# Performance work log

Hardware: AMD Instinct MI355X
Metric: run time of the kernel (lower is better)

Reference implementation:

```python
import jax, jax.numpy as jnp
import numpy as np

D = 256       # hp.encoder_dim
F = 256       # hp.duration_predictor_filter_size
K = 3         # hp.duration_predictor_kernel_size
ALPHA = 1.0
EPS = 1e-5


def _conv1d(x, w):
    # x: [N, L, Cin], w: [K, Cin, Cout], 'same' padding=1 for K=3
    return jax.lax.conv_general_dilated(
        x, w, window_strides=(1,), padding=((1, 1),),
        dimension_numbers=('NWC', 'WIO', 'NWC'))


def _layer_norm(h, g, b):
    mu = jnp.mean(h, axis=-1, keepdims=True)
    var = jnp.var(h, axis=-1, keepdims=True)
    return (h - mu) * jax.lax.rsqrt(var + EPS) * g + b


def setup_inputs() -> dict:
    key = jax.random.key(0)
    ks = jax.random.split(key, 12)
    N, L = 16, 512
    xavier_cw = float(np.sqrt(2.0 / (D * K + F * K)))  # xavier-ish for conv
    xavier_lw = float(np.sqrt(2.0 / (F + 1)))
    return {
        'x': jax.random.normal(ks[0], (N, L, D), dtype=jnp.float32),
        'conv1_w': jax.random.normal(ks[1], (K, D, F), dtype=jnp.float32) * xavier_cw,
        'conv1_b': jnp.zeros((F,), dtype=jnp.float32),
        'ln1_g': jnp.ones((F,), dtype=jnp.float32),
        'ln1_b': jnp.zeros((F,), dtype=jnp.float32),
        'conv2_w': jax.random.normal(ks[2], (K, F, F), dtype=jnp.float32) * xavier_cw,
        'conv2_b': jnp.zeros((F,), dtype=jnp.float32),
        'ln2_g': jnp.ones((F,), dtype=jnp.float32),
        'ln2_b': jnp.zeros((F,), dtype=jnp.float32),
        'lin_w': jax.random.normal(ks[3], (F, 1), dtype=jnp.float32) * xavier_lw,
        'lin_b': jnp.zeros((1,), dtype=jnp.float32),
        'WVF_max_length': 4096,
    }


def reference(x, conv1_w, conv1_b, ln1_g, ln1_b, conv2_w, conv2_b,
              ln2_g, ln2_b, lin_w, lin_b, WVF_max_length):
    # ---- DurationPredictor (eval mode: dropout = identity) ----
    h = _conv1d(x, conv1_w) + conv1_b            # [N, L, F]
    h = jax.nn.relu(_layer_norm(h, ln1_g, ln1_b))
    h = _conv1d(h, conv2_w) + conv2_b
    h = jax.nn.relu(_layer_norm(h, ln2_g, ln2_b))
    dpo = jax.nn.relu(h @ lin_w + lin_b)[..., 0]  # [N, L]

    # ---- LengthRegulator (no attn): int durations, alignment @ x ----
    dur = ((dpo + 0.5) * ALPHA).astype(jnp.int32)  # [N, L]
    ends = jnp.cumsum(dur, axis=-1)                # inclusive cumsum
    starts = ends - dur                            # exclusive cumsum
    t = jnp.arange(WVF_max_length)                 # static output length
    # alignment[n, t, l] = 1 iff starts[n,l] <= t < ends[n,l]
    align = ((t[None, :, None] >= starts[:, None, :]) &
             (t[None, :, None] < ends[:, None, :])).astype(x.dtype)  # [N, T, L]
    out = jnp.einsum('ntl,nld->ntd', align, x)     # [N, T, D]

    WVF_pos = jnp.arange(1, WVF_max_length + 1, dtype=jnp.int64
                         if jax.config.jax_enable_x64 else jnp.int32)[None, :]
    return out, WVF_pos
```

## Files before the change

kernel.cpp:

```cpp
#include <hip/hip_runtime.h>
#include <math.h>

#define N_   16
#define L_   512
#define C_   256
#define T_   4096
#define EPSL 1e-5f
#define BM   32

typedef short short8 __attribute__((ext_vector_type(8)));
typedef float f32x4  __attribute__((ext_vector_type(4)));

__device__ __forceinline__ ushort f2bf(float f) {
    union { float f; unsigned u; } v; v.f = f;
    return (ushort)((v.u + 0x7FFF + ((v.u >> 16) & 1)) >> 16);
}

__global__ __launch_bounds__(256) void pack_w_kernel(
    const float* __restrict__ w1, const float* __restrict__ w2,
    ushort* __restrict__ bpk1, ushort* __restrict__ bpk2,
    float* __restrict__ wpos)
{
    int gid = blockIdx.x * 256 + threadIdx.x;
    if (gid < T_) wpos[gid] = (float)(gid + 1);
    const float* w  = (gid < 24576) ? w1 : w2;
    ushort* bpk     = (gid < 24576) ? bpk1 : bpk2;
    int g2 = gid & 24575;
    int lane = g2 & 63;
    int s    = (g2 >> 6) & 7;
    int cg   = (g2 >> 9) & 15;
    int karm = g2 >> 13;
    int cin0 = s * 32 + (lane >> 4) * 8;
    int cout = cg * 16 + (lane & 15);
    const float* src = w + (size_t)(karm * 256 + cin0) * 256 + cout;
    short8 o;
    #pragma unroll
    for (int e = 0; e < 8; ++e) o[e] = (short)f2bf(src[(size_t)e * 256]);
    *reinterpret_cast<short8*>(bpk + (size_t)g2 * 8) = o;
}

__global__ __launch_bounds__(512, 4) void fused_conv_kernel(
    const float* __restrict__ x,
    const ushort* __restrict__ bpk1, const ushort* __restrict__ bpk2,
    const float* __restrict__ b1, const float* __restrict__ g1, const float* __restrict__ be1,
    const float* __restrict__ b2, const float* __restrict__ g2, const float* __restrict__ be2,
    const float* __restrict__ lw, const float* __restrict__ lb,
    int* __restrict__ dur)
{
    __shared__ __align__(16) char xt[50 * 512];
    __shared__ __align__(16) char h1t[34 * 512];
    __shared__ float redS[8][48], redQ[8][48], redP[8][32];

    const int tid  = threadIdx.x;
    const int wv   = tid >> 6;
    const int lane = tid & 63;
    const int lg   = lane >> 4;
    const int lr   = lane & 15;
    const int n    = blockIdx.x >> 4;
    const int l0   = (blockIdx.x & 15) << 5;
    const int cg0  = wv * 2;
    const int col0 = wv * 32 + lr, col1 = col0 + 16;

    for (int idx = tid; idx < 36 * 32; idx += 512) {
        int r = idx >> 5, slot = idx & 31;
        int l = l0 - 2 + r;
        short8 vb = {0,0,0,0,0,0,0,0};
        if (l >= 0 && l < L_) {
            const float* src = x + (((size_t)(n * L_ + l)) << 8) + (slot << 3);
            f32x4 f0 = *reinterpret_cast<const f32x4*>(src);
            f32x4 f1 = *reinterpret_cast<const f32x4*>(src + 4);
            vb[0]=(short)f2bf(f0[0]); vb[1]=(short)f2bf(f0[1]);
            vb[2]=(short)f2bf(f0[2]); vb[3]=(short)f2bf(f0[3]);
            vb[4]=(short)f2bf(f1[0]); vb[5]=(short)f2bf(f1[1]);
            vb[6]=(short)f2bf(f1[2]); vb[7]=(short)f2bf(f1[3]);
        }
        *reinterpret_cast<short8*>(xt + r * 512 + ((slot ^ (r & 15)) << 4)) = vb;
    }
    __syncthreads();

    f32x4 a1t[3][2] = {};
    #pragma unroll
    for (int karm = 0; karm < 3; ++karm) {
        const ushort* bb = bpk1 + ((size_t)(karm * 16 + cg0)) * 4096 + lane * 8;
        #pragma unroll
        for (int half = 0; half < 2; ++half) {
            short8 bf0[4], bf1[4];
            #pragma unroll
            for (int s4 = 0; s4 < 4; ++s4) {
                int s = half * 4 + s4;
                bf0[s4] = *reinterpret_cast<const short8*>(bb + s * 512);
                bf1[s4] = *reinterpret_cast<const short8*>(bb + 4096 + s * 512);
            }
            #pragma unroll
            for (int s4 = 0; s4 < 4; ++s4) {
                int s = half * 4 + s4;
                #pragma unroll
                for (int t = 0; t < 3; ++t) {
                    int rA = 16 * t + lr + karm;
                    short8 a = *reinterpret_cast<const short8*>(
                        xt + rA * 512 + ((((s << 2) + lg) ^ (rA & 15)) << 4));
                    a1t[t][0] = __builtin_amdgcn_mfma_f32_16x16x32_bf16(a, bf0[s4], a1t[t][0], 0, 0, 0);
                    a1t[t][1] = __builtin_amdgcn_mfma_f32_16x16x32_bf16(a, bf1[s4], a1t[t][1], 0, 0, 0);
                }
            }
        }
    }

    const float cb10 = b1[col0], cb11 = b1[col1];
    const float cg10 = g1[col0], cg11 = g1[col1];
    const float ce10 = be1[col0], ce11 = be1[col1];
    {
        float sv[12], qv[12];
        #pragma unroll
        for (int t = 0; t < 3; ++t)
            #pragma unroll
            for (int j = 0; j < 4; ++j) {
                float h0 = a1t[t][0][j] + cb10, h1 = a1t[t][1][j] + cb11;
                sv[t*4+j] = h0 + h1; qv[t*4+j] = h0 * h0 + h1 * h1;
            }
        #pragma unroll
        for (int m = 1; m < 16; m <<= 1)
            #pragma unroll
            for (int k = 0; k < 12; ++k) {
                sv[k] += __shfl_xor(sv[k], m, 64);
                qv[k] += __shfl_xor(qv[k], m, 64);
            }
        if (lr == 0) {
            #pragma unroll
            for (int t = 0; t < 3; ++t)
                #pragma unroll
                for (int j = 0; j < 4; ++j) {
                    redS[wv][16*t + lg*4 + j] = sv[t*4+j];
                    redQ[wv][16*t + lg*4 + j] = qv[t*4+j];
                }
        }
    }
    __syncthreads();
    if (tid < 48) {
        float ss = 0.f, qq = 0.f;
        #pragma unroll
        for (int u = 0; u < 8; ++u) { ss += redS[u][tid]; qq += redQ[u][tid]; }
        float m_  = ss * (1.f / 256.f);
        float var = fmaxf(qq * (1.f / 256.f) - m_ * m_, 0.f);
        redS[0][tid] = m_;
        redQ[0][tid] = 1.0f / sqrtf(var + EPSL);
    }
    __syncthreads();

    #pragma unroll
    for (int t = 0; t < 3; ++t)
        #pragma unroll
        for (int j = 0; j < 4; ++j) {
            int hr = 16*t + lg*4 + j;
            if (hr < 34) {
                int hl = l0 - 1 + hr;
                float r0 = 0.f, r1 = 0.f;
                if (hl >= 0 && hl < L_) {
                    r0 = fmaxf((a1t[t][0][j] + cb10 - redS[0][hr]) * redQ[0][hr] * cg10 + ce10, 0.f);
                    r1 = fmaxf((a1t[t][1][j] + cb11 - redS[0][hr]) * redQ[0][hr] * cg11 + ce11, 0.f);
                }
                *(ushort*)(h1t + hr*512 + (((col0 >> 3) ^ (hr & 15)) << 4) + (col0 & 7) * 2) = f2bf(r0);
                *(ushort*)(h1t + hr*512 + (((col1 >> 3) ^ (hr & 15)) << 4) + (col1 & 7) * 2) = f2bf(r1);
            }
        }
    __syncthreads();

    f32x4 c2[2][2] = {};
    #pragma unroll
    for (int karm = 0; karm < 3; ++karm) {
        const ushort* bb = bpk2 + ((size_t)(karm * 16 + cg0)) * 4096 + lane * 8;
        #pragma unroll
        for (int half = 0; half < 2; ++half) {
            short8 bf0[4], bf1[4];
            #pragma unroll
            for (int s4 = 0; s4 < 4; ++s4) {
                int s = half * 4 + s4;
                bf0[s4] = *reinterpret_cast<const short8*>(bb + s * 512);
                bf1[s4] = *reinterpret_cast<const short8*>(bb + 4096 + s * 512);
            }
            #pragma unroll
            for (int s4 = 0; s4 < 4; ++s4) {
                int s = half * 4 + s4;
                #pragma unroll
                for (int tt = 0; tt < 2; ++tt) {
                    int rA = 16 * tt + lr + karm;
                    short8 a = *reinterpret_cast<const short8*>(
                        h1t + rA * 512 + ((((s << 2) + lg) ^ (rA & 15)) << 4));
                    c2[tt][0] = __builtin_amdgcn_mfma_f32_16x16x32_bf16(a, bf0[s4], c2[tt][0], 0, 0, 0);
                    c2[tt][1] = __builtin_amdgcn_mfma_f32_16x16x32_bf16(a, bf1[s4], c2[tt][1], 0, 0, 0);
                }
            }
        }
    }

    const float cb20 = b2[col0], cb21 = b2[col1];
    const float cg20 = g2[col0], cg21 = g2[col1];
    const float ce20 = be2[col0], ce21 = be2[col1];
    const float lw0  = lw[col0],  lw1  = lw[col1];
    {
        float sv[8], qv[8];
        #pragma unroll
        for (int tt = 0; tt < 2; ++tt)
            #pragma unroll
            for (int j = 0; j < 4; ++j) {
                float h0 = c2[tt][0][j] + cb20, h1 = c2[tt][1][j] + cb21;
                sv[tt*4+j] = h0 + h1; qv[tt*4+j] = h0 * h0 + h1 * h1;
            }
        #pragma unroll
        for (int m = 1; m < 16; m <<= 1)
            #pragma unroll
            for (int k = 0; k < 8; ++k) {
                sv[k] += __shfl_xor(sv[k], m, 64);
                qv[k] += __shfl_xor(qv[k], m, 64);
            }
        if (lr == 0) {
            #pragma unroll
            for (int tt = 0; tt < 2; ++tt)
                #pragma unroll
                for (int j = 0; j < 4; ++j) {
                    redS[wv][16*tt + lg*4 + j] = sv[tt*4+j];
                    redQ[wv][16*tt + lg*4 + j] = qv[tt*4+j];
                }
        }
    }
    __syncthreads();
    if (tid < 32) {
        float ss = 0.f, qq = 0.f;
        #pragma unroll
        for (int u = 0; u < 8; ++u) { ss += redS[u][tid]; qq += redQ[u][tid]; }
        float m_  = ss * (1.f / 256.f);
        float var = fmaxf(qq * (1.f / 256.f) - m_ * m_, 0.f);
        redS[0][tid] = m_;
        redQ[0][tid] = 1.0f / sqrtf(var + EPSL);
    }
    __syncthreads();

    {
        float pv[8];
        #pragma unroll
        for (int tt = 0; tt < 2; ++tt)
            #pragma unroll
            for (int j = 0; j < 4; ++j) {
                int r = 16*tt + lg*4 + j;
                float r0 = fmaxf((c2[tt][0][j] + cb20 - redS[0][r]) * redQ[0][r] * cg20 + ce20, 0.f);
                float r1 = fmaxf((c2[tt][1][j] + cb21 - redS[0][r]) * redQ[0][r] * cg21 + ce21, 0.f);
                pv[tt*4+j] = r0 * lw0 + r1 * lw1;
            }
        #pragma unroll
        for (int m = 1; m < 16; m <<= 1)
            #pragma unroll
            for (int k = 0; k < 8; ++k)
                pv[k] += __shfl_xor(pv[k], m, 64);
        if (lr == 0) {
            #pragma unroll
            for (int tt = 0; tt < 2; ++tt)
                #pragma unroll
                for (int j = 0; j < 4; ++j)
                    redP[wv][16*tt + lg*4 + j] = pv[tt*4+j];
        }
    }
    __syncthreads();
    if (tid < 32) {
        float dot = lb[0];
        #pragma unroll
        for (int u = 0; u < 8; ++u) dot += redP[u][tid];
        dur[n * L_ + l0 + tid] = (int)(fmaxf(dot, 0.f) + 0.5f);
    }
}

__global__ __launch_bounds__(512) void gather_kernel(
    const float* __restrict__ x, const int* __restrict__ dur,
    float* __restrict__ out)
{
    __shared__ __align__(16) int se[L_];
    const int wid = threadIdx.x >> 6, lane = threadIdx.x & 63;
    const int blk = blockIdx.x;
    const int n = blk >> 9;

    if (wid == 0) {
        const int* dsrc = dur + n * L_;
        int4 va = reinterpret_cast<const int4*>(dsrc)[lane * 2];
        int4 vb = reinterpret_cast<const int4*>(dsrc)[lane * 2 + 1];
        int p0 = va.x,      p1 = p0 + va.y, p2 = p1 + va.z, p3 = p2 + va.w;
        int p4 = p3 + vb.x, p5 = p4 + vb.y, p6 = p5 + vb.z, p7 = p6 + vb.w;
        int tot = p7;
        #pragma unroll
        for (int m = 1; m < 64; m <<= 1) {
            int tu = __shfl_up(tot, m, 64);
            if (lane >= m) tot += tu;
        }
        int off = tot - p7;
        reinterpret_cast<int4*>(se)[lane * 2]     = make_int4(p0+off, p1+off, p2+off, p3+off);
        reinterpret_cast<int4*>(se)[lane * 2 + 1] = make_int4(p4+off, p5+off, p6+off, p7+off);
    }
    __syncthreads();

    const int t = ((blk & 511) << 3) + wid;
    const int total = se[L_ - 1];

    f32x4 v = {0.f, 0.f, 0.f, 0.f};
    if (t < total) {
        int p = 0;
        #pragma unroll
        for (int step = 256; step > 0; step >>= 1)
            if (p + step <= L_ && se[p + step - 1] <= t) p += step;
        v = reinterpret_cast<const f32x4*>(x + (((size_t)(n * L_ + p)) << 8))[lane];
    }
    __builtin_nontemporal_store(
        v, reinterpret_cast<f32x4*>(out + (((size_t)(n * T_ + t)) << 8)) + lane);
}

extern "C" void kernel_launch(void* const* d_in, const int* in_sizes, int n_in,
                              void* d_out, int out_size, void* d_ws, size_t ws_size,
                              hipStream_t stream)
{
    const float* x   = (const float*)d_in[0];
    const float* w1  = (const float*)d_in[1];
    const float* b1  = (const float*)d_in[2];
    const float* g1  = (const float*)d_in[3];
    const float* be1 = (const float*)d_in[4];
    const float* w2  = (const float*)d_in[5];
    const float* b2  = (const float*)d_in[6];
    const float* g2  = (const float*)d_in[7];
    const float* be2 = (const float*)d_in[8];
    const float* lw  = (const float*)d_in[9];
    const float* lb  = (const float*)d_in[10];

    float* out = (float*)d_out;
    ushort* bpk1 = (ushort*)d_out;
    ushort* bpk2 = bpk1 + 196608;
    int* dur     = (int*)d_ws;

    pack_w_kernel<<<192, 256, 0, stream>>>(w1, w2, bpk1, bpk2,
                                           out + (size_t)N_ * T_ * C_);

    fused_conv_kernel<<<N_ * (L_ / BM), 512, 0, stream>>>(
        x, bpk1, bpk2, b1, g1, be1, b2, g2, be2, lw, lb, dur);

    gather_kernel<<<N_ * T_ / 8, 512, 0, stream>>>(x, dur, out);
}
```

Before: 41.21 us.

## Double-buffer conv weight fragments in registers across kernel taps and layers

Weight B-fragments for each kernel tap are now loaded one tap ahead into two 16-entry register buffers, so global/L2 loads overlap the MFMA work of the previous tap and even the LayerNorm stage between the two convolutions. The first tap's weights are prefetched before the input tile is staged into LDS. The occupancy hint in the launch bounds is dropped to allow the much larger register footprint, at the cost of fewer resident waves per CU.

```diff
diff --git a/kernel.cpp b/kernel.cpp
--- a/kernel.cpp
+++ b/kernel.cpp
@@ -39,7 +39,39 @@
     *reinterpret_cast<short8*>(bpk + (size_t)g2 * 8) = o;
 }
 
-__global__ __launch_bounds__(512, 4) void fused_conv_kernel(
+#define LDB(BPK, KARM, DST) do {                                              \
+    const ushort* bb_ = (BPK) + ((size_t)((KARM) * 16 + cg0)) * 4096 + lane * 8; \
+    _Pragma("unroll")                                                         \
+    for (int s_ = 0; s_ < 8; ++s_) {                                          \
+        DST[s_]     = *reinterpret_cast<const short8*>(bb_ + s_ * 512);       \
+        DST[8 + s_] = *reinterpret_cast<const short8*>(bb_ + 4096 + s_ * 512);\
+    } } while (0)
+
+#define CONV1K(KARM, B) do {                                                  \
+    _Pragma("unroll")                                                         \
+    for (int s_ = 0; s_ < 8; ++s_) {                                          \
+        _Pragma("unroll")                                                     \
+        for (int t_ = 0; t_ < 3; ++t_) {                                      \
+            int rA_ = 16 * t_ + lr + (KARM);                                  \
+            short8 a_ = *reinterpret_cast<const short8*>(                     \
+                xt + rA_ * 512 + ((((s_ << 2) + lg) ^ (rA_ & 15)) << 4));     \
+            acc1[t_][0] = __builtin_amdgcn_mfma_f32_16x16x32_bf16(a_, B[s_],     acc1[t_][0], 0, 0, 0); \
+            acc1[t_][1] = __builtin_amdgcn_mfma_f32_16x16x32_bf16(a_, B[8 + s_], acc1[t_][1], 0, 0, 0); \
+        } } } while (0)
+
+#define CONV2K(KARM, B) do {                                                  \
+    _Pragma("unroll")                                                         \
+    for (int s_ = 0; s_ < 8; ++s_) {                                          \
+        _Pragma("unroll")                                                     \
+        for (int t_ = 0; t_ < 2; ++t_) {                                      \
+            int rA_ = 16 * t_ + lr + (KARM);                                  \
+            short8 a_ = *reinterpret_cast<const short8*>(                     \
+                h1t + rA_ * 512 + ((((s_ << 2) + lg) ^ (rA_ & 15)) << 4));    \
+            c2[t_][0] = __builtin_amdgcn_mfma_f32_16x16x32_bf16(a_, B[s_],     c2[t_][0], 0, 0, 0); \
+            c2[t_][1] = __builtin_amdgcn_mfma_f32_16x16x32_bf16(a_, B[8 + s_], c2[t_][1], 0, 0, 0); \
+        } } } while (0)
+
+__global__ __launch_bounds__(512) void fused_conv_kernel(
     const float* __restrict__ x,
     const ushort* __restrict__ bpk1, const ushort* __restrict__ bpk2,
     const float* __restrict__ b1, const float* __restrict__ g1, const float* __restrict__ be1,
@@ -60,6 +92,9 @@
     const int l0   = (blockIdx.x & 15) << 5;
     const int cg0  = wv * 2;
     const int col0 = wv * 32 + lr, col1 = col0 + 16;
+
+    short8 Ba[16], Bb[16];
+    LDB(bpk1, 0, Ba);
 
     for (int idx = tid; idx < 36 * 32; idx += 512) {
         int r = idx >> 5, slot = idx & 31;
@@ -78,33 +113,11 @@
     }
     __syncthreads();
 
-    f32x4 a1t[3][2] = {};
-    #pragma unroll
-    for (int karm = 0; karm < 3; ++karm) {
-        const ushort* bb = bpk1 + ((size_t)(karm * 16 + cg0)) * 4096 + lane * 8;
-        #pragma unroll
-        for (int half = 0; half < 2; ++half) {
-            short8 bf0[4], bf1[4];
-            #pragma unroll
-            for (int s4 = 0; s4 < 4; ++s4) {
-                int s = half * 4 + s4;
-                bf0[s4] = *reinterpret_cast<const short8*>(bb + s * 512);
-                bf1[s4] = *reinterpret_cast<const short8*>(bb + 4096 + s * 512);
-            }
-            #pragma unroll
-            for (int s4 = 0; s4 < 4; ++s4) {
-                int s = half * 4 + s4;
-                #pragma unroll
-                for (int t = 0; t < 3; ++t) {
-                    int rA = 16 * t + lr + karm;
-                    short8 a = *reinterpret_cast<const short8*>(
-                        xt + rA * 512 + ((((s << 2) + lg) ^ (rA & 15)) << 4));
-                    a1t[t][0] = __builtin_amdgcn_mfma_f32_16x16x32_bf16(a, bf0[s4], a1t[t][0], 0, 0, 0);
-                    a1t[t][1] = __builtin_amdgcn_mfma_f32_16x16x32_bf16(a, bf1[s4], a1t[t][1], 0, 0, 0);
-                }
-            }
-        }
-    }
+    f32x4 acc1[3][2] = {};
+    LDB(bpk1, 1, Bb);  CONV1K(0, Ba);
+    LDB(bpk1, 2, Ba);  CONV1K(1, Bb);
+    LDB(bpk2, 0, Bb);  CONV1K(2, Ba);
+    LDB(bpk2, 1, Ba);
 
     const float cb10 = b1[col0], cb11 = b1[col1];
     const float cg10 = g1[col0], cg11 = g1[col1];
@@ -115,7 +128,7 @@
         for (int t = 0; t < 3; ++t)
             #pragma unroll
             for (int j = 0; j < 4; ++j) {
-                float h0 = a1t[t][0][j] + cb10, h1 = a1t[t][1][j] + cb11;
+                float h0 = acc1[t][0][j] + cb10, h1 = acc1[t][1][j] + cb11;
                 sv[t*4+j] = h0 + h1; qv[t*4+j] = h0 * h0 + h1 * h1;
             }
         #pragma unroll
@@ -156,8 +169,8 @@
                 int hl = l0 - 1 + hr;
                 float r0 = 0.f, r1 = 0.f;
                 if (hl >= 0 && hl < L_) {
-                    r0 = fmaxf((a1t[t][0][j] + cb10 - redS[0][hr]) * redQ[0][hr] * cg10 + ce10, 0.f);
-                    r1 = fmaxf((a1t[t][1][j] + cb11 - redS[0][hr]) * redQ[0][hr] * cg11 + ce11, 0.f);
+                    r0 = fmaxf((acc1[t][0][j] + cb10 - redS[0][hr]) * redQ[0][hr] * cg10 + ce10, 0.f);
+                    r1 = fmaxf((acc1[t][1][j] + cb11 - redS[0][hr]) * redQ[0][hr] * cg11 + ce11, 0.f);
                 }
                 *(ushort*)(h1t + hr*512 + (((col0 >> 3) ^ (hr & 15)) << 4) + (col0 & 7) * 2) = f2bf(r0);
                 *(ushort*)(h1t + hr*512 + (((col1 >> 3) ^ (hr & 15)) << 4) + (col1 & 7) * 2) = f2bf(r1);
@@ -166,32 +179,9 @@
     __syncthreads();
 
     f32x4 c2[2][2] = {};
-    #pragma unroll
-    for (int karm = 0; karm < 3; ++karm) {
-        const ushort* bb = bpk2 + ((size_t)(karm * 16 + cg0)) * 4096 + lane * 8;
-        #pragma unroll
-        for (int half = 0; half < 2; ++half) {
-            short8 bf0[4], bf1[4];
-            #pragma unroll
-            for (int s4 = 0; s4 < 4; ++s4) {
-                int s = half * 4 + s4;
-                bf0[s4] = *reinterpret_cast<const short8*>(bb + s * 512);
-                bf1[s4] = *reinterpret_cast<const short8*>(bb + 4096 + s * 512);
-            }
-            #pragma unroll
-            for (int s4 = 0; s4 < 4; ++s4) {
-                int s = half * 4 + s4;
-                #pragma unroll
-                for (int tt = 0; tt < 2; ++tt) {
-                    int rA = 16 * tt + lr + karm;
-                    short8 a = *reinterpret_cast<const short8*>(
-                        h1t + rA * 512 + ((((s << 2) + lg) ^ (rA & 15)) << 4));
-                    c2[tt][0] = __builtin_amdgcn_mfma_f32_16x16x32_bf16(a, bf0[s4], c2[tt][0], 0, 0, 0);
-                    c2[tt][1] = __builtin_amdgcn_mfma_f32_16x16x32_bf16(a, bf1[s4], c2[tt][1], 0, 0, 0);
-                }
-            }
-        }
-    }
+    CONV2K(0, Bb);  LDB(bpk2, 2, Bb);
+    CONV2K(1, Ba);
+    CONV2K(2, Bb);
 
     const float cb20 = b2[col0], cb21 = b2[col1];
     const float cg20 = g2[col0], cg21 = g2[col1];
```

New measurement: 38.73 us. -6.0%, faster.
